# Kernel tuning notes

Measured on AMD Instinct MI355X. Metric: run time of the kernel, lower is better.

The kernel has to match this reference:

```python
import jax, jax.numpy as jnp
import numpy as np

EMBED = 256
HEADS = 8
GROUP = 64
HEAD_DIM = EMBED // HEADS
N = 131072

def setup_inputs() -> dict:
    key = jax.random.key(0)
    k1, k2, k3 = jax.random.split(key, 3)
    s_in = 1.0 / np.sqrt(EMBED)
    x = jax.random.normal(k1, (N, EMBED), dtype=jnp.float32)
    w_qkv = jax.random.normal(k2, (3 * EMBED, EMBED), dtype=jnp.float32) * s_in  # nn.Linear weight [out,in]
    w_out = jax.random.normal(k3, (EMBED, EMBED), dtype=jnp.float32) * s_in
    b_out = jnp.zeros((EMBED,), dtype=jnp.float32)
    return {"x": x, "w_qkv": w_qkv, "w_out": w_out, "b_out": b_out}

def reference(x, w_qkv, w_out, b_out):
    Ntok, C = x.shape
    ng = Ntok // GROUP  # number of groups
    qkv = x @ w_qkv.T                      # (N, 3C)
    qkv = qkv.reshape(Ntok, 3, C)
    q, k, v = qkv[:, 0], qkv[:, 1], qkv[:, 2]

    def to_heads(t):
        # '(n g) (h c) -> (n h) g c'
        t = t.reshape(ng, GROUP, HEADS, HEAD_DIM)
        return t.transpose(0, 2, 1, 3).reshape(ng * HEADS, GROUP, HEAD_DIM)

    q, k, v = to_heads(q), to_heads(k), to_heads(v)
    # grouped attention over local windows of size GROUP
    energy = jnp.einsum('nqd,nkd->nqk', q, k)           # (n*h, g, g)
    attn = jax.nn.softmax(energy / jnp.sqrt(jnp.float32(C)), axis=-1)  # scale by sqrt(embed_size), as in source
    out = jnp.einsum('nql,nld->nqd', attn, v)           # (n*h, g, hd)
    # '(n h) g c -> (n g) (h c)'
    out = out.reshape(ng, HEADS, GROUP, HEAD_DIM).transpose(0, 2, 1, 3).reshape(Ntok, C)
    return out @ w_out.T + b_out
```

## Files before the change

### kernel.cpp

```cpp
#include <hip/hip_runtime.h>
#include <hip/hip_bf16.h>
#include <stdint.h>

typedef __attribute__((ext_vector_type(8))) short s16x8;
typedef __attribute__((ext_vector_type(4))) float f32x4;

__device__ __forceinline__ unsigned short f32_bf16(float f) {
  union { float f; uint32_t u; } v; v.f = f;
  return (unsigned short)((v.u + 0x7FFFu + ((v.u >> 16) & 1u)) >> 16);
}

__device__ __forceinline__ uint32_t pack_bf16(float lo, float hi) {
  __hip_bfloat162 h = __float22bfloat162_rn(float2{lo, hi});
  union { __hip_bfloat162 h; uint32_t u; } u; u.h = h; return u.u;
}

__device__ __forceinline__ s16x8 xchg(uint32_t lo0, uint32_t lo1,
                                      uint32_t hi0, uint32_t hi1,
                                      int srcA, int srcB, uint32_t hisel) {
  int a0 = __shfl((int)lo0, srcA), b0 = __shfl((int)hi0, srcA);
  int a1 = __shfl((int)lo1, srcA), b1 = __shfl((int)hi1, srcA);
  int a2 = __shfl((int)lo0, srcB), b2 = __shfl((int)hi0, srcB);
  int a3 = __shfl((int)lo1, srcB), b3 = __shfl((int)hi1, srcB);
  union { uint32_t u[4]; s16x8 v; } r;
  r.u[0] = hisel ? (uint32_t)b0 : (uint32_t)a0;
  r.u[1] = hisel ? (uint32_t)b1 : (uint32_t)a1;
  r.u[2] = hisel ? (uint32_t)b2 : (uint32_t)a2;
  r.u[3] = hisel ? (uint32_t)b3 : (uint32_t)a3;
  return r.v;
}

__global__ void convert_w(const float* __restrict__ wqkv,
                          const float* __restrict__ wout,
                          unsigned short* __restrict__ o) {
  int i = blockIdx.x * 256 + threadIdx.x;
  if (i < 768 * 256) o[i] = f32_bf16(wqkv[i]);
  else               o[i] = f32_bf16(wout[i - 768 * 256]);
}

__global__ __launch_bounds__(512, 2) void mha_fused(
    const float* __restrict__ x,
    const unsigned short* __restrict__ wqkv,
    const unsigned short* __restrict__ wout,
    const float* __restrict__ bias,
    float* __restrict__ out) {
  __shared__ unsigned short xt[64 * 256];

  const int g    = blockIdx.x;
  const int tid  = threadIdx.x;
  const int h    = tid >> 6;
  const int lane = tid & 63;
  const int l15  = lane & 15;
  const int l4   = lane >> 4;

  {
    const int row = tid >> 3;
    const int c0  = (tid & 7) * 32;
    const float* src = x + (size_t)(g * 64 + row) * 256 + c0;
    const uint32_t swz = (uint32_t)(row & 7) << 4;
#pragma unroll
    for (int c = 0; c < 32; c += 8) {
      float4 f0 = *(const float4*)(src + c);
      float4 f1 = *(const float4*)(src + c + 4);
      uint32_t p0 = pack_bf16(f0.x, f0.y);
      uint32_t p1 = pack_bf16(f0.z, f0.w);
      uint32_t p2 = pack_bf16(f1.x, f1.y);
      uint32_t p3 = pack_bf16(f1.z, f1.w);
      uint32_t byte = ((uint32_t)(row * 512 + (c0 + c) * 2)) ^ swz;
      *(uint4*)((char*)xt + byte) = make_uint4(p0, p1, p2, p3);
    }
  }
  __syncthreads();

  const uint32_t swz   = (uint32_t)(l15 & 7) << 4;
  const int      srcA  = l15 + ((lane & 16) << 1);
  const int      srcB  = srcA + 16;
  const uint32_t hisel = (uint32_t)(lane & 32);

  const unsigned short* wbase = wqkv + (size_t)(h * 32 + l15) * 256 + l4 * 8;

  f32x4 qT[2][4], kT[2][4];
#pragma unroll
  for (int t = 0; t < 2; ++t)
#pragma unroll
    for (int m = 0; m < 4; ++m) {
      qT[t][m] = (f32x4){0.f, 0.f, 0.f, 0.f};
      kT[t][m] = (f32x4){0.f, 0.f, 0.f, 0.f};
    }

  for (int kk = 0; kk < 8; ++kk) {
    s16x8 a[4];
#pragma unroll
    for (int m = 0; m < 4; ++m) {
      uint32_t byte = ((uint32_t)((16 * m + l15) * 512 + kk * 64 + l4 * 16)) ^ swz;
      a[m] = *(const s16x8*)((const char*)xt + byte);
    }
#pragma unroll
    for (int t = 0; t < 2; ++t) {
      const unsigned short* wp = wbase + (size_t)(16 * t) * 256 + kk * 32;
      s16x8 wq = *(const s16x8*)(wp);
      s16x8 wk = *(const s16x8*)(wp + 256 * 256);
#pragma unroll
      for (int m = 0; m < 4; ++m) {
        qT[t][m] = __builtin_amdgcn_mfma_f32_16x16x32_bf16(wq, a[m], qT[t][m], 0, 0, 0);
        kT[t][m] = __builtin_amdgcn_mfma_f32_16x16x32_bf16(wk, a[m], kT[t][m], 0, 0, 0);
      }
    }
  }

  s16x8 kA[4], qB[4];
#pragma unroll
  for (int m = 0; m < 4; ++m) {
    uint32_t q00 = pack_bf16(qT[0][m][0], qT[0][m][1]);
    uint32_t q01 = pack_bf16(qT[0][m][2], qT[0][m][3]);
    uint32_t q10 = pack_bf16(qT[1][m][0], qT[1][m][1]);
    uint32_t q11 = pack_bf16(qT[1][m][2], qT[1][m][3]);
    qB[m] = xchg(q00, q01, q10, q11, srcA, srcB, hisel);
    uint32_t k00 = pack_bf16(kT[0][m][0], kT[0][m][1]);
    uint32_t k01 = pack_bf16(kT[0][m][2], kT[0][m][3]);
    uint32_t k10 = pack_bf16(kT[1][m][0], kT[1][m][1]);
    uint32_t k11 = pack_bf16(kT[1][m][2], kT[1][m][3]);
    kA[m] = xchg(k00, k01, k10, k11, srcA, srcB, hisel);
  }

  uint32_t pkP[4][4][2];
#pragma unroll
  for (int n = 0; n < 4; ++n) {
    f32x4 en[4];
#pragma unroll
    for (int m = 0; m < 4; ++m) {
      en[m] = (f32x4){0.f, 0.f, 0.f, 0.f};
      en[m] = __builtin_amdgcn_mfma_f32_16x16x32_bf16(kA[m], qB[n], en[m], 0, 0, 0);
    }
    float mx = en[0][0];
#pragma unroll
    for (int m = 0; m < 4; ++m)
#pragma unroll
      for (int r = 0; r < 4; ++r) mx = fmaxf(mx, en[m][r]);
    mx = fmaxf(mx, __shfl_xor(mx, 16));
    mx = fmaxf(mx, __shfl_xor(mx, 32));
    float p[4][4];
    float sum = 0.f;
#pragma unroll
    for (int m = 0; m < 4; ++m)
#pragma unroll
      for (int r = 0; r < 4; ++r) {
        float t = __expf((en[m][r] - mx) * 0.0625f);
        p[m][r] = t;
        sum += t;
      }
    sum += __shfl_xor(sum, 16);
    sum += __shfl_xor(sum, 32);
    float rs = 1.0f / sum;
#pragma unroll
    for (int m = 0; m < 4; ++m) {
      pkP[n][m][0] = pack_bf16(p[m][0] * rs, p[m][1] * rs);
      pkP[n][m][1] = pack_bf16(p[m][2] * rs, p[m][3] * rs);
    }
  }

  f32x4 vv[4][2];
#pragma unroll
  for (int m = 0; m < 4; ++m) {
    vv[m][0] = (f32x4){0.f, 0.f, 0.f, 0.f};
    vv[m][1] = (f32x4){0.f, 0.f, 0.f, 0.f};
  }
  for (int kk = 0; kk < 8; ++kk) {
    s16x8 a[4];
#pragma unroll
    for (int m = 0; m < 4; ++m) {
      uint32_t byte = ((uint32_t)((16 * m + l15) * 512 + kk * 64 + l4 * 16)) ^ swz;
      a[m] = *(const s16x8*)((const char*)xt + byte);
    }
    const unsigned short* wp = wbase + (size_t)512 * 256 + kk * 32;
    s16x8 wv0 = *(const s16x8*)(wp);
    s16x8 wv1 = *(const s16x8*)(wp + 16 * 256);
#pragma unroll
    for (int m = 0; m < 4; ++m) {
      vv[m][0] = __builtin_amdgcn_mfma_f32_16x16x32_bf16(a[m], wv0, vv[m][0], 0, 0, 0);
      vv[m][1] = __builtin_amdgcn_mfma_f32_16x16x32_bf16(a[m], wv1, vv[m][1], 0, 0, 0);
    }
  }
  uint32_t pkV[2][4][2];
#pragma unroll
  for (int t = 0; t < 2; ++t)
#pragma unroll
    for (int m = 0; m < 4; ++m) {
      pkV[t][m][0] = pack_bf16(vv[m][t][0], vv[m][t][1]);
      pkV[t][m][1] = pack_bf16(vv[m][t][2], vv[m][t][3]);
    }

  f32x4 o[4][2];
#pragma unroll
  for (int nb = 0; nb < 4; ++nb) {
    o[nb][0] = (f32x4){0.f, 0.f, 0.f, 0.f};
    o[nb][1] = (f32x4){0.f, 0.f, 0.f, 0.f};
  }
#pragma unroll
  for (int kk2 = 0; kk2 < 2; ++kk2) {
    s16x8 vB[2];
#pragma unroll
    for (int t = 0; t < 2; ++t)
      vB[t] = xchg(pkV[t][2 * kk2][0], pkV[t][2 * kk2][1],
                   pkV[t][2 * kk2 + 1][0], pkV[t][2 * kk2 + 1][1], srcA, srcB, hisel);
#pragma unroll
    for (int nb = 0; nb < 4; ++nb) {
      s16x8 pA = xchg(pkP[nb][2 * kk2][0], pkP[nb][2 * kk2][1],
                      pkP[nb][2 * kk2 + 1][0], pkP[nb][2 * kk2 + 1][1], srcA, srcB, hisel);
      o[nb][0] = __builtin_amdgcn_mfma_f32_16x16x32_bf16(pA, vB[0], o[nb][0], 0, 0, 0);
      o[nb][1] = __builtin_amdgcn_mfma_f32_16x16x32_bf16(pA, vB[1], o[nb][1], 0, 0, 0);
    }
  }

  __syncthreads();
#pragma unroll
  for (int nb = 0; nb < 4; ++nb)
#pragma unroll
    for (int t = 0; t < 2; ++t)
#pragma unroll
      for (int r = 0; r < 4; ++r) {
        int row = 16 * nb + 4 * l4 + r;
        int col = h * 32 + 16 * t + l15;
        uint32_t byte = ((uint32_t)(row * 512 + col * 2)) ^ ((uint32_t)(row & 7) << 4);
        *(unsigned short*)((char*)xt + byte) = f32_bf16(o[nb][t][r]);
      }
  __syncthreads();

  f32x4 acc[4][2];
#pragma unroll
  for (int m = 0; m < 4; ++m) {
    acc[m][0] = (f32x4){0.f, 0.f, 0.f, 0.f};
    acc[m][1] = (f32x4){0.f, 0.f, 0.f, 0.f};
  }
  const unsigned short* wobase = wout + (size_t)(h * 32 + l15) * 256 + l4 * 8;
  for (int kk = 0; kk < 8; ++kk) {
    s16x8 a[4];
#pragma unroll
    for (int m = 0; m < 4; ++m) {
      uint32_t byte = ((uint32_t)((16 * m + l15) * 512 + kk * 64 + l4 * 16)) ^ swz;
      a[m] = *(const s16x8*)((const char*)xt + byte);
    }
    s16x8 wo0 = *(const s16x8*)(wobase + kk * 32);
    s16x8 wo1 = *(const s16x8*)(wobase + (size_t)16 * 256 + kk * 32);
#pragma unroll
    for (int m = 0; m < 4; ++m) {
      acc[m][0] = __builtin_amdgcn_mfma_f32_16x16x32_bf16(a[m], wo0, acc[m][0], 0, 0, 0);
      acc[m][1] = __builtin_amdgcn_mfma_f32_16x16x32_bf16(a[m], wo1, acc[m][1], 0, 0, 0);
    }
  }

  const float b0 = bias[h * 32 + l15];
  const float b1 = bias[h * 32 + 16 + l15];
  float* dst = out + (size_t)g * 64 * 256 + h * 32;
#pragma unroll
  for (int m = 0; m < 4; ++m)
#pragma unroll
    for (int r = 0; r < 4; ++r) {
      int tok = 16 * m + 4 * l4 + r;
      dst[(size_t)tok * 256 + l15]      = acc[m][0][r] + b0;
      dst[(size_t)tok * 256 + 16 + l15] = acc[m][1][r] + b1;
    }
}

extern "C" void kernel_launch(void* const* d_in, const int* in_sizes, int n_in,
                              void* d_out, int out_size, void* d_ws, size_t ws_size,
                              hipStream_t stream) {
  const float* x    = (const float*)d_in[0];
  const float* wqkv = (const float*)d_in[1];
  const float* wout = (const float*)d_in[2];
  const float* bout = (const float*)d_in[3];
  float* out = (float*)d_out;

  unsigned short* wq_bf = (unsigned short*)d_ws;
  unsigned short* wo_bf = wq_bf + 768 * 256;

  convert_w<<<1024, 256, 0, stream>>>(wqkv, wout, wq_bf);
  mha_fused<<<2048, 512, 0, stream>>>(x, wq_bf, wo_bf, bout, out);
}
```

Baseline: 209.1 us.

## Halve block to four waves, each processing two heads sequentially

Reduces the block from 512 to 256 threads, so each wave loops over two heads instead of one. The attention is restructured so softmax and P·V run per query block, which drops the large pkP register array and should lower register pressure. A second shared buffer holds the first-half head outputs, so the second pass can write into the x tile only after a barrier. The output projection then runs in two passes per wave. This trades less per-block parallelism and more serial work per wave for lower register pressure and possibly higher occupancy, at the cost of 16 KB more shared memory per block.

```diff
diff --git a/kernel.cpp b/kernel.cpp
--- a/kernel.cpp
+++ b/kernel.cpp
@@ -38,35 +38,36 @@
   else               o[i] = f32_bf16(wout[i - 768 * 256]);
 }
 
-__global__ __launch_bounds__(512, 2) void mha_fused(
+__global__ __launch_bounds__(256, 2) void mha_fused(
     const float* __restrict__ x,
     const unsigned short* __restrict__ wqkv,
     const unsigned short* __restrict__ wout,
     const float* __restrict__ bias,
     float* __restrict__ out) {
   __shared__ unsigned short xt[64 * 256];
+  __shared__ unsigned short ot0[64 * 128];
 
   const int g    = blockIdx.x;
   const int tid  = threadIdx.x;
-  const int h    = tid >> 6;
+  const int w    = tid >> 6;
   const int lane = tid & 63;
   const int l15  = lane & 15;
   const int l4   = lane >> 4;
 
   {
-    const int row = tid >> 3;
-    const int c0  = (tid & 7) * 32;
-    const float* src = x + (size_t)(g * 64 + row) * 256 + c0;
-    const uint32_t swz = (uint32_t)(row & 7) << 4;
-#pragma unroll
-    for (int c = 0; c < 32; c += 8) {
-      float4 f0 = *(const float4*)(src + c);
-      float4 f1 = *(const float4*)(src + c + 4);
+    const int rr = tid >> 5;
+    const int cc = (tid & 31) * 8;
+#pragma unroll
+    for (int it = 0; it < 8; ++it) {
+      int row = rr + 8 * it;
+      const float* src = x + (size_t)(g * 64 + row) * 256 + cc;
+      float4 f0 = *(const float4*)(src);
+      float4 f1 = *(const float4*)(src + 4);
       uint32_t p0 = pack_bf16(f0.x, f0.y);
       uint32_t p1 = pack_bf16(f0.z, f0.w);
       uint32_t p2 = pack_bf16(f1.x, f1.y);
       uint32_t p3 = pack_bf16(f1.z, f1.w);
-      uint32_t byte = ((uint32_t)(row * 512 + (c0 + c) * 2)) ^ swz;
+      uint32_t byte = ((uint32_t)(row * 512 + cc * 2)) ^ ((uint32_t)(row & 7) << 4);
       *(uint4*)((char*)xt + byte) = make_uint4(p0, p1, p2, p3);
     }
   }
@@ -77,189 +78,200 @@
   const int      srcB  = srcA + 16;
   const uint32_t hisel = (uint32_t)(lane & 32);
 
-  const unsigned short* wbase = wqkv + (size_t)(h * 32 + l15) * 256 + l4 * 8;
-
-  f32x4 qT[2][4], kT[2][4];
-#pragma unroll
-  for (int t = 0; t < 2; ++t)
-#pragma unroll
-    for (int m = 0; m < 4; ++m) {
-      qT[t][m] = (f32x4){0.f, 0.f, 0.f, 0.f};
-      kT[t][m] = (f32x4){0.f, 0.f, 0.f, 0.f};
-    }
-
-  for (int kk = 0; kk < 8; ++kk) {
-    s16x8 a[4];
-#pragma unroll
-    for (int m = 0; m < 4; ++m) {
-      uint32_t byte = ((uint32_t)((16 * m + l15) * 512 + kk * 64 + l4 * 16)) ^ swz;
-      a[m] = *(const s16x8*)((const char*)xt + byte);
-    }
-#pragma unroll
-    for (int t = 0; t < 2; ++t) {
-      const unsigned short* wp = wbase + (size_t)(16 * t) * 256 + kk * 32;
-      s16x8 wq = *(const s16x8*)(wp);
-      s16x8 wk = *(const s16x8*)(wp + 256 * 256);
-#pragma unroll
-      for (int m = 0; m < 4; ++m) {
-        qT[t][m] = __builtin_amdgcn_mfma_f32_16x16x32_bf16(wq, a[m], qT[t][m], 0, 0, 0);
-        kT[t][m] = __builtin_amdgcn_mfma_f32_16x16x32_bf16(wk, a[m], kT[t][m], 0, 0, 0);
-      }
-    }
-  }
-
-  s16x8 kA[4], qB[4];
-#pragma unroll
-  for (int m = 0; m < 4; ++m) {
-    uint32_t q00 = pack_bf16(qT[0][m][0], qT[0][m][1]);
-    uint32_t q01 = pack_bf16(qT[0][m][2], qT[0][m][3]);
-    uint32_t q10 = pack_bf16(qT[1][m][0], qT[1][m][1]);
-    uint32_t q11 = pack_bf16(qT[1][m][2], qT[1][m][3]);
-    qB[m] = xchg(q00, q01, q10, q11, srcA, srcB, hisel);
-    uint32_t k00 = pack_bf16(kT[0][m][0], kT[0][m][1]);
-    uint32_t k01 = pack_bf16(kT[0][m][2], kT[0][m][3]);
-    uint32_t k10 = pack_bf16(kT[1][m][0], kT[1][m][1]);
-    uint32_t k11 = pack_bf16(kT[1][m][2], kT[1][m][3]);
-    kA[m] = xchg(k00, k01, k10, k11, srcA, srcB, hisel);
-  }
-
-  uint32_t pkP[4][4][2];
-#pragma unroll
-  for (int n = 0; n < 4; ++n) {
-    f32x4 en[4];
-#pragma unroll
-    for (int m = 0; m < 4; ++m) {
-      en[m] = (f32x4){0.f, 0.f, 0.f, 0.f};
-      en[m] = __builtin_amdgcn_mfma_f32_16x16x32_bf16(kA[m], qB[n], en[m], 0, 0, 0);
-    }
-    float mx = en[0][0];
-#pragma unroll
-    for (int m = 0; m < 4; ++m)
-#pragma unroll
-      for (int r = 0; r < 4; ++r) mx = fmaxf(mx, en[m][r]);
-    mx = fmaxf(mx, __shfl_xor(mx, 16));
-    mx = fmaxf(mx, __shfl_xor(mx, 32));
-    float p[4][4];
-    float sum = 0.f;
-#pragma unroll
-    for (int m = 0; m < 4; ++m)
-#pragma unroll
-      for (int r = 0; r < 4; ++r) {
-        float t = __expf((en[m][r] - mx) * 0.0625f);
-        p[m][r] = t;
-        sum += t;
-      }
-    sum += __shfl_xor(sum, 16);
-    sum += __shfl_xor(sum, 32);
-    float rs = 1.0f / sum;
-#pragma unroll
-    for (int m = 0; m < 4; ++m) {
-      pkP[n][m][0] = pack_bf16(p[m][0] * rs, p[m][1] * rs);
-      pkP[n][m][1] = pack_bf16(p[m][2] * rs, p[m][3] * rs);
-    }
-  }
-
-  f32x4 vv[4][2];
-#pragma unroll
-  for (int m = 0; m < 4; ++m) {
-    vv[m][0] = (f32x4){0.f, 0.f, 0.f, 0.f};
-    vv[m][1] = (f32x4){0.f, 0.f, 0.f, 0.f};
-  }
-  for (int kk = 0; kk < 8; ++kk) {
-    s16x8 a[4];
-#pragma unroll
-    for (int m = 0; m < 4; ++m) {
-      uint32_t byte = ((uint32_t)((16 * m + l15) * 512 + kk * 64 + l4 * 16)) ^ swz;
-      a[m] = *(const s16x8*)((const char*)xt + byte);
-    }
-    const unsigned short* wp = wbase + (size_t)512 * 256 + kk * 32;
-    s16x8 wv0 = *(const s16x8*)(wp);
-    s16x8 wv1 = *(const s16x8*)(wp + 16 * 256);
-#pragma unroll
-    for (int m = 0; m < 4; ++m) {
-      vv[m][0] = __builtin_amdgcn_mfma_f32_16x16x32_bf16(a[m], wv0, vv[m][0], 0, 0, 0);
-      vv[m][1] = __builtin_amdgcn_mfma_f32_16x16x32_bf16(a[m], wv1, vv[m][1], 0, 0, 0);
-    }
-  }
-  uint32_t pkV[2][4][2];
-#pragma unroll
-  for (int t = 0; t < 2; ++t)
-#pragma unroll
-    for (int m = 0; m < 4; ++m) {
-      pkV[t][m][0] = pack_bf16(vv[m][t][0], vv[m][t][1]);
-      pkV[t][m][1] = pack_bf16(vv[m][t][2], vv[m][t][3]);
-    }
-
-  f32x4 o[4][2];
-#pragma unroll
-  for (int nb = 0; nb < 4; ++nb) {
-    o[nb][0] = (f32x4){0.f, 0.f, 0.f, 0.f};
-    o[nb][1] = (f32x4){0.f, 0.f, 0.f, 0.f};
-  }
-#pragma unroll
-  for (int kk2 = 0; kk2 < 2; ++kk2) {
-    s16x8 vB[2];
-#pragma unroll
-    for (int t = 0; t < 2; ++t)
-      vB[t] = xchg(pkV[t][2 * kk2][0], pkV[t][2 * kk2][1],
-                   pkV[t][2 * kk2 + 1][0], pkV[t][2 * kk2 + 1][1], srcA, srcB, hisel);
+#pragma unroll 1
+  for (int hh = 0; hh < 2; ++hh) {
+    const int h = w + 4 * hh;
+    const unsigned short* wbase = wqkv + (size_t)(h * 32 + l15) * 256 + l4 * 8;
+
+    s16x8 qB[4], kA[4];
+    {
+      f32x4 qT[2][4], kT[2][4];
+#pragma unroll
+      for (int t = 0; t < 2; ++t)
+#pragma unroll
+        for (int m = 0; m < 4; ++m) {
+          qT[t][m] = (f32x4){0.f, 0.f, 0.f, 0.f};
+          kT[t][m] = (f32x4){0.f, 0.f, 0.f, 0.f};
+        }
+      for (int kk = 0; kk < 8; ++kk) {
+        s16x8 a[4];
+#pragma unroll
+        for (int m = 0; m < 4; ++m) {
+          uint32_t byte = ((uint32_t)((16 * m + l15) * 512 + kk * 64 + l4 * 16)) ^ swz;
+          a[m] = *(const s16x8*)((const char*)xt + byte);
+        }
+#pragma unroll
+        for (int t = 0; t < 2; ++t) {
+          s16x8 wq = *(const s16x8*)(wbase + (size_t)(16 * t) * 256 + kk * 32);
+          s16x8 wk = *(const s16x8*)(wbase + (size_t)(256 + 16 * t) * 256 + kk * 32);
+#pragma unroll
+          for (int m = 0; m < 4; ++m) {
+            qT[t][m] = __builtin_amdgcn_mfma_f32_16x16x32_bf16(wq, a[m], qT[t][m], 0, 0, 0);
+            kT[t][m] = __builtin_amdgcn_mfma_f32_16x16x32_bf16(wk, a[m], kT[t][m], 0, 0, 0);
+          }
+        }
+      }
+#pragma unroll
+      for (int m = 0; m < 4; ++m) {
+        qB[m] = xchg(pack_bf16(qT[0][m][0], qT[0][m][1]), pack_bf16(qT[0][m][2], qT[0][m][3]),
+                     pack_bf16(qT[1][m][0], qT[1][m][1]), pack_bf16(qT[1][m][2], qT[1][m][3]),
+                     srcA, srcB, hisel);
+        kA[m] = xchg(pack_bf16(kT[0][m][0], kT[0][m][1]), pack_bf16(kT[0][m][2], kT[0][m][3]),
+                     pack_bf16(kT[1][m][0], kT[1][m][1]), pack_bf16(kT[1][m][2], kT[1][m][3]),
+                     srcA, srcB, hisel);
+      }
+    }
+
+    s16x8 vB[2][2];
+    {
+      f32x4 vv[4][2];
+#pragma unroll
+      for (int m = 0; m < 4; ++m) {
+        vv[m][0] = (f32x4){0.f, 0.f, 0.f, 0.f};
+        vv[m][1] = (f32x4){0.f, 0.f, 0.f, 0.f};
+      }
+      for (int kk = 0; kk < 8; ++kk) {
+        s16x8 a[4];
+#pragma unroll
+        for (int m = 0; m < 4; ++m) {
+          uint32_t byte = ((uint32_t)((16 * m + l15) * 512 + kk * 64 + l4 * 16)) ^ swz;
+          a[m] = *(const s16x8*)((const char*)xt + byte);
+        }
+        const unsigned short* wp = wbase + (size_t)512 * 256 + kk * 32;
+        s16x8 wv0 = *(const s16x8*)(wp);
+        s16x8 wv1 = *(const s16x8*)(wp + 16 * 256);
+#pragma unroll
+        for (int m = 0; m < 4; ++m) {
+          vv[m][0] = __builtin_amdgcn_mfma_f32_16x16x32_bf16(a[m], wv0, vv[m][0], 0, 0, 0);
+          vv[m][1] = __builtin_amdgcn_mfma_f32_16x16x32_bf16(a[m], wv1, vv[m][1], 0, 0, 0);
+        }
+      }
+      uint32_t pkv[2][4][2];
+#pragma unroll
+      for (int t = 0; t < 2; ++t)
+#pragma unroll
+        for (int m = 0; m < 4; ++m) {
+          pkv[t][m][0] = pack_bf16(vv[m][t][0], vv[m][t][1]);
+          pkv[t][m][1] = pack_bf16(vv[m][t][2], vv[m][t][3]);
+        }
+#pragma unroll
+      for (int kk2 = 0; kk2 < 2; ++kk2)
+#pragma unroll
+        for (int t = 0; t < 2; ++t)
+          vB[kk2][t] = xchg(pkv[t][2 * kk2][0], pkv[t][2 * kk2][1],
+                            pkv[t][2 * kk2 + 1][0], pkv[t][2 * kk2 + 1][1],
+                            srcA, srcB, hisel);
+    }
+
+    if (hh == 1) __syncthreads();
+
 #pragma unroll
     for (int nb = 0; nb < 4; ++nb) {
-      s16x8 pA = xchg(pkP[nb][2 * kk2][0], pkP[nb][2 * kk2][1],
-                      pkP[nb][2 * kk2 + 1][0], pkP[nb][2 * kk2 + 1][1], srcA, srcB, hisel);
-      o[nb][0] = __builtin_amdgcn_mfma_f32_16x16x32_bf16(pA, vB[0], o[nb][0], 0, 0, 0);
-      o[nb][1] = __builtin_amdgcn_mfma_f32_16x16x32_bf16(pA, vB[1], o[nb][1], 0, 0, 0);
-    }
-  }
-
-  __syncthreads();
-#pragma unroll
-  for (int nb = 0; nb < 4; ++nb)
-#pragma unroll
-    for (int t = 0; t < 2; ++t)
+      f32x4 en[4];
+#pragma unroll
+      for (int m = 0; m < 4; ++m) {
+        en[m] = (f32x4){0.f, 0.f, 0.f, 0.f};
+        en[m] = __builtin_amdgcn_mfma_f32_16x16x32_bf16(kA[m], qB[nb], en[m], 0, 0, 0);
+      }
+      float mx = en[0][0];
+#pragma unroll
+      for (int m = 0; m < 4; ++m)
+#pragma unroll
+        for (int r = 0; r < 4; ++r) mx = fmaxf(mx, en[m][r]);
+      mx = fmaxf(mx, __shfl_xor(mx, 16));
+      mx = fmaxf(mx, __shfl_xor(mx, 32));
+      float p[4][4];
+      float sum = 0.f;
+#pragma unroll
+      for (int m = 0; m < 4; ++m)
+#pragma unroll
+        for (int r = 0; r < 4; ++r) {
+          float t = __expf((en[m][r] - mx) * 0.0625f);
+          p[m][r] = t;
+          sum += t;
+        }
+      sum += __shfl_xor(sum, 16);
+      sum += __shfl_xor(sum, 32);
+      float rs = 1.0f / sum;
+      uint32_t pk[4][2];
+#pragma unroll
+      for (int m = 0; m < 4; ++m) {
+        pk[m][0] = pack_bf16(p[m][0] * rs, p[m][1] * rs);
+        pk[m][1] = pack_bf16(p[m][2] * rs, p[m][3] * rs);
+      }
+      f32x4 o0 = (f32x4){0.f, 0.f, 0.f, 0.f};
+      f32x4 o1 = (f32x4){0.f, 0.f, 0.f, 0.f};
+#pragma unroll
+      for (int kk2 = 0; kk2 < 2; ++kk2) {
+        s16x8 pA = xchg(pk[2 * kk2][0], pk[2 * kk2][1],
+                        pk[2 * kk2 + 1][0], pk[2 * kk2 + 1][1], srcA, srcB, hisel);
+        o0 = __builtin_amdgcn_mfma_f32_16x16x32_bf16(pA, vB[kk2][0], o0, 0, 0, 0);
+        o1 = __builtin_amdgcn_mfma_f32_16x16x32_bf16(pA, vB[kk2][1], o1, 0, 0, 0);
+      }
 #pragma unroll
       for (int r = 0; r < 4; ++r) {
         int row = 16 * nb + 4 * l4 + r;
-        int col = h * 32 + 16 * t + l15;
-        uint32_t byte = ((uint32_t)(row * 512 + col * 2)) ^ ((uint32_t)(row & 7) << 4);
-        *(unsigned short*)((char*)xt + byte) = f32_bf16(o[nb][t][r]);
-      }
+        uint32_t rsw = (uint32_t)(row & 7) << 4;
+        if (hh == 0) {
+          uint32_t b0 = ((uint32_t)(row * 256 + (w * 32 + l15) * 2)) ^ rsw;
+          uint32_t b1 = ((uint32_t)(row * 256 + (w * 32 + 16 + l15) * 2)) ^ rsw;
+          *(unsigned short*)((char*)ot0 + b0) = f32_bf16(o0[r]);
+          *(unsigned short*)((char*)ot0 + b1) = f32_bf16(o1[r]);
+        } else {
+          uint32_t b0 = ((uint32_t)(row * 512 + (128 + w * 32 + l15) * 2)) ^ rsw;
+          uint32_t b1 = ((uint32_t)(row * 512 + (128 + w * 32 + 16 + l15) * 2)) ^ rsw;
+          *(unsigned short*)((char*)xt + b0) = f32_bf16(o0[r]);
+          *(unsigned short*)((char*)xt + b1) = f32_bf16(o1[r]);
+        }
+      }
+    }
+  }
   __syncthreads();
 
-  f32x4 acc[4][2];
-#pragma unroll
-  for (int m = 0; m < 4; ++m) {
-    acc[m][0] = (f32x4){0.f, 0.f, 0.f, 0.f};
-    acc[m][1] = (f32x4){0.f, 0.f, 0.f, 0.f};
+#pragma unroll 1
+  for (int pp = 0; pp < 2; ++pp) {
+    const int colbase = 128 * pp + w * 32;
+    const unsigned short* wobase = wout + (size_t)(colbase + l15) * 256 + l4 * 8;
+    f32x4 acc[4][2];
+#pragma unroll
+    for (int m = 0; m < 4; ++m) {
+      acc[m][0] = (f32x4){0.f, 0.f, 0.f, 0.f};
+      acc[m][1] = (f32x4){0.f, 0.f, 0.f, 0.f};
+    }
+#pragma unroll
+    for (int kk = 0; kk < 8; ++kk) {
+      s16x8 a[4];
+#pragma unroll
+      for (int m = 0; m < 4; ++m) {
+        int row = 16 * m + l15;
+        if (kk < 4) {
+          uint32_t byte = ((uint32_t)(row * 256 + kk * 64 + l4 * 16)) ^ swz;
+          a[m] = *(const s16x8*)((const char*)ot0 + byte);
+        } else {
+          uint32_t byte = ((uint32_t)(row * 512 + kk * 64 + l4 * 16)) ^ swz;
+          a[m] = *(const s16x8*)((const char*)xt + byte);
+        }
+      }
+      s16x8 wo0 = *(const s16x8*)(wobase + kk * 32);
+      s16x8 wo1 = *(const s16x8*)(wobase + (size_t)16 * 256 + kk * 32);
+#pragma unroll
+      for (int m = 0; m < 4; ++m) {
+        acc[m][0] = __builtin_amdgcn_mfma_f32_16x16x32_bf16(a[m], wo0, acc[m][0], 0, 0, 0);
+        acc[m][1] = __builtin_amdgcn_mfma_f32_16x16x32_bf16(a[m], wo1, acc[m][1], 0, 0, 0);
+      }
+    }
+    const float b0 = bias[colbase + l15];
+    const float b1 = bias[colbase + 16 + l15];
+    float* dst = out + (size_t)g * 64 * 256 + colbase;
+#pragma unroll
+    for (int m = 0; m < 4; ++m)
+#pragma unroll
+      for (int r = 0; r < 4; ++r) {
+        int tok = 16 * m + 4 * l4 + r;
+        dst[(size_t)tok * 256 + l15]      = acc[m][0][r] + b0;
+        dst[(size_t)tok * 256 + 16 + l15] = acc[m][1][r] + b1;
+      }
   }
-  const unsigned short* wobase = wout + (size_t)(h * 32 + l15) * 256 + l4 * 8;
-  for (int kk = 0; kk < 8; ++kk) {
-    s16x8 a[4];
-#pragma unroll
-    for (int m = 0; m < 4; ++m) {
-      uint32_t byte = ((uint32_t)((16 * m + l15) * 512 + kk * 64 + l4 * 16)) ^ swz;
-      a[m] = *(const s16x8*)((const char*)xt + byte);
-    }
-    s16x8 wo0 = *(const s16x8*)(wobase + kk * 32);
-    s16x8 wo1 = *(const s16x8*)(wobase + (size_t)16 * 256 + kk * 32);
-#pragma unroll
-    for (int m = 0; m < 4; ++m) {
-      acc[m][0] = __builtin_amdgcn_mfma_f32_16x16x32_bf16(a[m], wo0, acc[m][0], 0, 0, 0);
-      acc[m][1] = __builtin_amdgcn_mfma_f32_16x16x32_bf16(a[m], wo1, acc[m][1], 0, 0, 0);
-    }
-  }
-
-  const float b0 = bias[h * 32 + l15];
-  const float b1 = bias[h * 32 + 16 + l15];
-  float* dst = out + (size_t)g * 64 * 256 + h * 32;
-#pragma unroll
-  for (int m = 0; m < 4; ++m)
-#pragma unroll
-    for (int r = 0; r < 4; ++r) {
-      int tok = 16 * m + 4 * l4 + r;
-      dst[(size_t)tok * 256 + l15]      = acc[m][0][r] + b0;
-      dst[(size_t)tok * 256 + 16 + l15] = acc[m][1][r] + b1;
-    }
 }
 
 extern "C" void kernel_launch(void* const* d_in, const int* in_sizes, int n_in,
@@ -275,5 +287,5 @@
   unsigned short* wo_bf = wq_bf + 768 * 256;
 
   convert_w<<<1024, 256, 0, stream>>>(wqkv, wout, wq_bf);
-  mha_fused<<<2048, 512, 0, stream>>>(x, wq_bf, wo_bf, bout, out);
-}
+  mha_fused<<<2048, 256, 0, stream>>>(x, wq_bf, wo_bf, bout, out);
+}
```

Result: slower. 242.9 us (+16.1%).
